# Kernel optimization log

Hardware: AMD Instinct MI355X
Metric: run time of the kernel (lower is better)

Reference implementation:

```python
import jax, jax.numpy as jnp
import numpy as np
from jax import lax

NUM_SUPERNODES = 1024
KNN_K = 16
MIN_GRIPPER = 16
MIN_MASK = 8
GRIP_START = 0
GRIP_RADIUS = 0.1
NEG_INF = -jnp.inf


def _take(a, idx):
    return jnp.take_along_axis(a, idx, axis=1)


def _scatter_or(idx, keep, Bf, N):
    # OR `keep` into a fresh [Bf,N] bool mask at positions idx (mirrors torch scatter_)
    b = jnp.arange(Bf)[:, None]
    return jnp.zeros((Bf, N), dtype=bool).at[b, idx].max(keep)


def _cdist(a, b):
    # a [B,M,3], b [B,N,3] -> [B,M,N] euclidean
    d2 = (jnp.sum(a * a, -1)[:, :, None] + jnp.sum(b * b, -1)[:, None, :]
          - 2.0 * jnp.einsum('bmd,bnd->bmn', a, b))
    return jnp.sqrt(jnp.maximum(d2, 0.0))


def _sample_supernodes(xyz, valid, state, mask_id, extra_scores, global_scores):
    Bf, N, _ = xyz.shape
    M = NUM_SUPERNODES
    valid = valid.astype(bool)
    row_has_valid = valid.any(axis=1)
    first_valid = jnp.argmax(valid, axis=1).astype(jnp.int32)  # [Bf]

    # ---- gripper quota: nearest points to gripper xyz (within radius if any) ----
    k_grip = min(MIN_GRIPPER, M)
    gxyz = state[:, GRIP_START:GRIP_START + 3]
    gdist = jnp.linalg.norm(xyz - gxyz[:, None, :], axis=-1)  # [Bf,N]
    in_radius = gdist <= GRIP_RADIUS
    has_radius = (valid & in_radius).any(axis=1, keepdims=True)
    eligible = valid & (in_radius | ~has_radius)
    dist_rank = jnp.where(eligible, gdist, jnp.inf)
    neg_vals, grip_idx = lax.top_k(-dist_rank, k_grip)
    grip_vals = -neg_vals
    grip_keep = jnp.isfinite(grip_vals) & row_has_valid[:, None]
    head_idx = jnp.where(grip_keep, grip_idx, first_valid[:, None])
    head_bucket = jnp.where(grip_keep, 1, -1)
    selected = _scatter_or(grip_idx, grip_keep, Bf, N)

    remaining = M - k_grip
    # ---- mask-instance quota: one point per mask id (dedup via sort) ----
    mask_cand = valid & ~selected
    sentinel = jnp.iinfo(mask_id.dtype).max
    mask_key = jnp.where(mask_cand, mask_id, sentinel)
    sort_idx = jnp.argsort(mask_key, axis=1)
    sorted_valid = _take(mask_cand, sort_idx)
    sorted_mask = _take(mask_id, sort_idx)
    first_for_id = jnp.concatenate(
        [sorted_valid[:, :1],
         sorted_valid[:, 1:] & (sorted_mask[:, 1:] != sorted_mask[:, :-1])], axis=1)
    pos = jnp.arange(N, dtype=jnp.float32)[None, :]
    mask_scores = jnp.where(first_for_id, -pos, NEG_INF)
    mask_vals, mask_pos = lax.top_k(mask_scores, remaining)
    mask_idx = _take(sort_idx, mask_pos)
    mask_keep = jnp.isfinite(mask_vals) & row_has_valid[:, None]
    selected_after_mask = selected | _scatter_or(mask_idx, mask_keep, Bf, N)

    # ---- extra random mask supernodes to guarantee min_mask quota ----
    k_extra = min(MIN_MASK, remaining)
    es = jnp.where(valid & ~selected_after_mask, extra_scores, NEG_INF)
    extra_vals, extra_idx = lax.top_k(es, k_extra)
    extra_keep = jnp.isfinite(extra_vals) & row_has_valid[:, None]
    use_extra = ~mask_keep[:, :k_extra] & extra_keep
    mask_idx = mask_idx.at[:, :k_extra].set(
        jnp.where(use_extra, extra_idx, mask_idx[:, :k_extra]))
    mask_keep = mask_keep.at[:, :k_extra].set(mask_keep[:, :k_extra] | use_extra)

    # ---- global random fill ----
    selected_for_global = selected | _scatter_or(mask_idx, mask_keep, Bf, N)
    gs = jnp.where(valid & ~selected_for_global, global_scores, NEG_INF)
    gvals, gidx = lax.top_k(gs, remaining)
    gkeep = jnp.isfinite(gvals) & row_has_valid[:, None]
    fill_idx = jnp.where(mask_keep, mask_idx,
                         jnp.where(gkeep, gidx, first_valid[:, None]))
    fill_bucket = jnp.where(mask_keep, 2, jnp.where(gkeep, 0, -1))

    out_idx = jnp.concatenate([head_idx, fill_idx], axis=1)
    out_bucket = jnp.concatenate([head_bucket, fill_bucket], axis=1)
    out_valid = _take(valid, out_idx) & row_has_valid[:, None]
    out_bucket = jnp.where(out_valid, out_bucket, -1)
    return out_idx, out_valid, out_bucket


def setup_inputs() -> dict:
    key = jax.random.key(0)
    ks = jax.random.split(key, 6)
    Bf, N, C = 8, 16384, 64
    return {
        'x': jax.random.normal(ks[0], (Bf, N, C), dtype=jnp.float32),
        'xyz': jax.random.normal(ks[1], (Bf, N, 3), dtype=jnp.float32),
        'valid': jnp.ones((Bf, N), dtype=bool),
        'state': jax.random.normal(ks[2], (Bf, 8), dtype=jnp.float32),
        'mask_id': jax.random.randint(ks[3], (Bf, N), 0, 32, dtype=jnp.int32),
        'extra_scores': jax.random.uniform(ks[4], (Bf, N), dtype=jnp.float32),
        'global_scores': jax.random.uniform(ks[5], (Bf, N), dtype=jnp.float32),
    }


def reference(x, xyz, valid, state, mask_id, extra_scores, global_scores):
    Bf, N, C = x.shape
    out_idx, out_valid, out_bucket = _sample_supernodes(
        xyz, valid, state, mask_id, extra_scores, global_scores)
    # gather_points
    supernode_xyz = _take(xyz, out_idx[:, :, None].repeat(3, axis=2))  # [Bf,M,3]
    # build_knn_neighbors: masked cdist + topk smallest
    dist = _cdist(supernode_xyz.astype(jnp.float32), xyz.astype(jnp.float32))
    dist = jnp.where(valid.astype(bool)[:, None, :], dist, jnp.inf)
    neg_vals, neighbor_idx = lax.top_k(-dist, KNN_K)
    neighbor_mask = jnp.isfinite(-neg_vals)  # [Bf,M,K]
    # gather_neighbors
    b = jnp.arange(Bf)[:, None, None]
    neighbor_feats = x[b, neighbor_idx]  # [Bf,M,K,C]
    return (neighbor_feats, supernode_xyz, neighbor_mask,
            out_idx, out_valid, out_bucket)
```

## Files before the change

kernel.cpp:

```cpp
#include <hip/hip_runtime.h>
#include <math.h>

typedef unsigned long long u64;
typedef unsigned int u32;

#define BF 8
#define NPTS 16384
#define HALFPTS 8192
#define M_SN 1024
#define CCH 64
#define KNN 16
#define NTHR1 1024
#define KPER 16
#define TBL 4096
#define CCAP 2048
#define REM 1008

constexpr size_t O0 = 0;
constexpr size_t O1 = 8388608;
constexpr size_t O2 = 8413184;
constexpr size_t O3 = 8544256;
constexpr size_t O4 = 8552448;
constexpr size_t O5 = 8560640;

#define PW_OFF ((size_t)256)
#define PW_BYTES ((size_t)BF * NPTS * 16)
#define WN_BYTES ((size_t)2 * BF * M_SN * KNN * 8)

__device__ __forceinline__ bool is_valid_el(const void* vp, int mode, long long i) {
  if (mode == 1) return ((const unsigned char*)vp)[i] != 0;
  if (mode == 2) return ((const float*)vp)[i] != 0.0f;
  return ((const int*)vp)[i] != 0;
}

__device__ __forceinline__ u32 desc_enc(float f) {
  u32 u = __float_as_uint(f);
  u32 s = (u & 0x80000000u) ? ~u : (u | 0x80000000u);
  return ~s;
}
__device__ __forceinline__ bool enc_finite(u32 d) {
  u32 s = ~d;
  u32 u = (s & 0x80000000u) ? (s & 0x7FFFFFFFu) : ~s;
  return (u & 0x7F800000u) != 0x7F800000u;
}

__device__ __forceinline__ u64 wave_min_u64(u64 v) {
#pragma unroll
  for (int d = 32; d >= 1; d >>= 1) {
    u32 lo = __shfl_xor((u32)(v & 0xFFFFFFFFu), d, 64);
    u32 hi = __shfl_xor((u32)(v >> 32), d, 64);
    u64 o = ((u64)hi << 32) | lo;
    if (o < v) v = o;
  }
  return v;
}

__device__ __forceinline__ u64 block_min_u64(u64 v, u64* red16, int t) {
  v = wave_min_u64(v);
  if ((t & 63) == 0) red16[t >> 6] = v;
  __syncthreads();
  if (t < 64) {
    u64 x = red16[t & 15];
    x = wave_min_u64(x);
    if (t == 0) red16[0] = x;
  }
  __syncthreads();
  u64 r = red16[0];
  __syncthreads();
  return r;
}

__device__ __forceinline__ int block_excl_scan(int val, int* scanb, int t, int* tot) {
  int incl = val;
#pragma unroll
  for (int d = 1; d < 64; d <<= 1) {
    int v = __shfl_up(incl, d, 64);
    if ((t & 63) >= d) incl += v;
  }
  if ((t & 63) == 63) scanb[t >> 6] = incl;
  __syncthreads();
  if (t < 64) {
    int ws = (t < 16) ? scanb[t] : 0;
#pragma unroll
    for (int d = 1; d < 16; d <<= 1) {
      int v = __shfl_up(ws, d, 64);
      if ((t & 63) >= d) ws += v;
    }
    if (t < 16) scanb[16 + t] = ws;
  }
  __syncthreads();
  int wv = t >> 6;
  int base = (wv == 0) ? 0 : scanb[16 + wv - 1];
  *tot = scanb[16 + 15];
  int r = base + incl - val;
  __syncthreads();
  return r;
}

__device__ __forceinline__ u64 shfl64_grp(u64 v, int src) {
  u32 lo = (u32)__shfl((int)(u32)(v & 0xFFFFFFFFu), src, 32);
  u32 hi = (u32)__shfl((int)(u32)(v >> 32), src, 32);
  return ((u64)hi << 32) | lo;
}

template<bool ASC, bool SHIFTBIN>
__device__ __forceinline__ void topk_select(const u32* ek, const u32* bk, u32 cmask,
    int Twant, int* table, u64* cand, int* scanb, int* sh, int* outArr, int t) {
  for (int j = t; j < TBL; j += NTHR1) table[j] = 0;
  if (t == 6) sh[6] = 0x7FFFFFFF;
  if (t == 7) sh[7] = 1;
  __syncthreads();
#pragma unroll
  for (int k = 0; k < KPER; k++) {
    if ((cmask >> k) & 1u) {
      int bin = SHIFTBIN ? (int)(ek[k] >> 20) : (int)bk[k];
      atomicAdd(&table[bin], 1);
    }
  }
  __syncthreads();
  int c_[4]; int c4 = 0;
#pragma unroll
  for (int q = 0; q < 4; q++) { c_[q] = table[4 * t + q]; c4 += c_[q]; }
  int htot;
  int cum = block_excl_scan(c4, scanb, t, &htot);
  const int T = min(Twant, htot);
  int e_ = cum;
#pragma unroll
  for (int q = 0; q < 4; q++) {
    int nx = e_ + c_[q];
    if (T > 0 && e_ < T && nx >= T) atomicMin(&sh[6], 4 * t + q);
    table[4 * t + q] = e_;
    e_ = nx;
  }
  __syncthreads();
  if (T <= 0) return;
  const int B = sh[6];
#pragma unroll
  for (int k = 0; k < KPER; k++) {
    if ((cmask >> k) & 1u) {
      int bin = SHIFTBIN ? (int)(ek[k] >> 20) : (int)bk[k];
      if (bin <= B) {
        int pos = atomicAdd(&table[bin], 1);
        if (pos < CCAP)
          cand[pos] = ((u64)ek[k] << 32) | ((u64)(u32)bin << 14) | (u32)(k * NTHR1 + t);
      }
    }
  }
  __syncthreads();
  const int nc = table[B];
  if (nc <= CCAP) {
    for (int c = t; c < nc; c += NTHR1) {
      u64 key = cand[c];
      int bin = (int)((key >> 14) & 0xFFFu);
      int s = bin ? table[bin - 1] : 0;
      int e2 = table[bin];
      int r = s;
      for (int j = s; j < e2; j++) r += (cand[j] < key);
      if (r < T) {
        u32 enc = (u32)(key >> 32);
        int ix = (int)(key & 0x3FFFu);
        bool fin = ASC ? (enc < 0x7F800000u) : enc_finite(enc);
        outArr[r] = fin ? ix : (ix | (int)0x80000000);
      }
    }
  } else {
    if (t == 0) sh[7] = 0;
  }
  __syncthreads();
}

__global__ void detect_valid(const unsigned* __restrict__ w, int nwords, int* __restrict__ flag) {
  int local = 0;
  for (int i = blockIdx.x * blockDim.x + threadIdx.x; i < nwords; i += gridDim.x * blockDim.x) {
    unsigned v = w[i];
    if (v == 0x3F800000u) local = 2;
    else if (v != 0u && v != 1u) local = max(local, 1);
  }
#pragma unroll
  for (int d = 32; d >= 1; d >>= 1) local = max(local, __shfl_xor(local, d, 64));
  if ((threadIdx.x & 63) == 0 && local) atomicMax(flag, local);
}

__global__ __launch_bounds__(1024)
void sample_kernel(const float* __restrict__ xyz, const void* __restrict__ validp,
                   const float* __restrict__ state, const int* __restrict__ mask_id,
                   const float* __restrict__ extra, const float* __restrict__ glob,
                   const int* __restrict__ flagp, float4* __restrict__ pw,
                   float* __restrict__ out) {
  __shared__ u64 red16[16];
  __shared__ int table[TBL];
  __shared__ int scanb[32];
  __shared__ int mpick[REM];
  __shared__ u64 cand[CCAP];
  __shared__ int gsorted[REM];
  __shared__ int head_i[16];
  __shared__ int head_bk[16];
  __shared__ int sh[8];

  const int b = blockIdx.x, t = threadIdx.x;
  const int vmode = flagp[0];
  const float* xyzb = xyz + (size_t)b * NPTS * 3;
  const int* midb = mask_id + (size_t)b * NPTS;
  const float* exb = extra + (size_t)b * NPTS;
  const float* glb = glob + (size_t)b * NPTS;

  if (t < 8) sh[t] = 0;
  if (t == 1) sh[1] = 0x7FFFFFFF;
  if (t < 16) gsorted[t] = -1;
  __syncthreads();

  u32 vbits = 0;
#pragma unroll
  for (int k = 0; k < KPER; k++) {
    int i = k * NTHR1 + t;
    if (is_valid_el(validp, vmode, (long long)b * NPTS + i)) vbits |= 1u << k;
  }
  if (vbits) {
    atomicOr(&sh[0], 1);
    atomicMin(&sh[1], (__ffs(vbits) - 1) * NTHR1 + t);
  }

  float gx = state[b * 8 + 0], gy = state[b * 8 + 1], gz = state[b * 8 + 2];
  float gd[KPER];
  u32 inr = 0;
#pragma unroll
  for (int k = 0; k < KPER; k++) {
    int i = k * NTHR1 + t;
    float px = xyzb[3 * i], py = xyzb[3 * i + 1], pz = xyzb[3 * i + 2];
    float dx = px - gx, dy = py - gy, dz = pz - gz;
    float d = sqrtf((dx * dx + dy * dy) + dz * dz);
    gd[k] = d;
    bool vb = (vbits >> k) & 1u;
    if (vb && d <= 0.1f) inr |= 1u << k;
    if (pw) {
      float sb = __fadd_rn(__fadd_rn(__fmul_rn(px, px), __fmul_rn(py, py)), __fmul_rn(pz, pz));
      pw[(size_t)b * NPTS + i] = make_float4(px, py, pz, vb ? sb : INFINITY);
    }
  }
  if (inr) atomicOr(&sh[2], 1);
  __syncthreads();

  const int rhv = sh[0];
  const int first_valid = rhv ? sh[1] : 0;
  const u32 elig = vbits & (sh[2] ? inr : 0xFFFFu);
  u32 sel = 0;

  {
    u32 ek[KPER];
#pragma unroll
    for (int k = 0; k < KPER; k++) ek[k] = __float_as_uint(gd[k]);
    topk_select<true, true>(ek, nullptr, elig, 16, table, cand, scanb, sh, gsorted, t);
    if (sh[7]) {
      if (t < 16) {
        int g = gsorted[t];
        head_i[t] = (g >= 0) ? g : first_valid;
        head_bk[t] = (g >= 0) ? 1 : -1;
      }
      __syncthreads();
      for (int j = 0; j < 16; j++) {
        if (head_bk[j] == 1) {
          int ix = head_i[j];
          if ((ix & (NTHR1 - 1)) == t) sel |= 1u << (ix >> 10);
        }
      }
    } else {
      for (int it = 0; it < 16; ++it) {
        u64 best = ~0ull;
#pragma unroll
        for (int k = 0; k < KPER; k++) {
          if (((elig >> k) & 1u) && !((sel >> k) & 1u)) {
            u64 key = ((u64)__float_as_uint(gd[k]) << 32) | (u32)(k * NTHR1 + t);
            if (key < best) best = key;
          }
        }
        u64 w = block_min_u64(best, red16, t);
        bool keep = (w >> 32) < 0x7F800000ull;
        int idx = (int)(w & 0xFFFFFFFFu);
        if (t == 0) { head_i[it] = keep ? idx : first_valid; head_bk[it] = keep ? 1 : -1; }
        if (keep && (idx & (NTHR1 - 1)) == t) sel |= 1u << (idx >> 10);
      }
      __syncthreads();
    }
  }

  for (int j = t; j < TBL; j += NTHR1) table[j] = 0x7FFFFFFF;
  __syncthreads();
#pragma unroll
  for (int k = 0; k < KPER; k++) {
    if (((vbits >> k) & 1u) && !((sel >> k) & 1u)) {
      int i = k * NTHR1 + t;
      int id = midb[i];
      if ((u32)id < TBL) atomicMin(&table[id], i);
    }
  }
  __syncthreads();
  int cnt = 0;
#pragma unroll
  for (int q = 0; q < 4; q++) cnt += (table[4 * t + q] != 0x7FFFFFFF);
  int mtot;
  int excl = block_excl_scan(cnt, scanb, t, &mtot);
  {
    int pos = excl;
#pragma unroll
    for (int q = 0; q < 4; q++) {
      int v = table[4 * t + q];
      if (v != 0x7FFFFFFF) { if (pos < REM) mpick[pos] = v; pos++; }
    }
  }
  __syncthreads();
  const int nm = min(mtot, REM);
  for (int j = 0; j < nm; j++) {
    int p = mpick[j];
    if ((p & (NTHR1 - 1)) == t) sel |= 1u << (p >> 10);
  }

  u32 extra_used = 0;
  if (nm < 8 && rhv) {
    u32 extrbits = 0;
    for (int j = 0; j < 8; j++) {
      u64 best = ~0ull;
#pragma unroll
      for (int k = 0; k < KPER; k++) {
        if (((vbits >> k) & 1u) && !((sel >> k) & 1u) && !((extrbits >> k) & 1u)) {
          int i = k * NTHR1 + t;
          u64 key = ((u64)desc_enc(exb[i]) << 32) | (u32)i;
          if (key < best) best = key;
        }
      }
      u64 w = block_min_u64(best, red16, t);
      if (w == ~0ull) break;
      int idx = (int)(w & 0xFFFFFFFFu);
      bool fin = enc_finite((u32)(w >> 32));
      if ((idx & (NTHR1 - 1)) == t) extrbits |= 1u << (idx >> 10);
      if (j >= nm && fin) {
        extra_used |= 1u << j;
        if (t == 0) mpick[j] = idx;
        if ((idx & (NTHR1 - 1)) == t) sel |= 1u << (idx >> 10);
      }
    }
    __syncthreads();
  }

  {
    u32 cbits = vbits & ~sel;
    u32 ek[KPER], bk[KPER];
#pragma unroll
    for (int k = 0; k < KPER; k++) {
      if ((cbits >> k) & 1u) {
        float f = glb[k * NTHR1 + t];
        ek[k] = desc_enc(f);
        float g = fminf(fmaxf(f, 0.0f), 0.99999994f);
        bk[k] = 4095u - (u32)(g * 4096.0f);
      } else { ek[k] = 0xFFFFFFFFu; bk[k] = 4095u; }
    }
    for (int j = t; j < REM; j += NTHR1) gsorted[j] = -1;
    topk_select<false, false>(ek, bk, cbits, REM, table, cand, scanb, sh, gsorted, t);
    if (!sh[7]) {
      u32 gext = 0;
      for (int j = 0; j < REM; j++) {
        u64 best = ~0ull;
#pragma unroll
        for (int k = 0; k < KPER; k++) {
          if (((cbits >> k) & 1u) && !((gext >> k) & 1u)) {
            u64 key = ((u64)ek[k] << 32) | (u32)(k * NTHR1 + t);
            if (key < best) best = key;
          }
        }
        u64 w = block_min_u64(best, red16, t);
        if (w == ~0ull) break;
        int idx = (int)(w & 0xFFFFFFFFu);
        if ((idx & (NTHR1 - 1)) == t) gext |= 1u << (idx >> 10);
        if (t == 0) gsorted[j] = enc_finite((u32)(w >> 32)) ? idx : (idx | (int)0x80000000);
      }
      __syncthreads();
    }
  }

  {
    int slot = t;
    int idx, bucket;
    if (slot < 16) {
      idx = head_i[slot];
      bucket = head_bk[slot];
    } else {
      int jj = slot - 16;
      bool mk = (jj < nm) || (jj < 8 && ((extra_used >> jj) & 1u));
      if (mk) { idx = mpick[jj]; bucket = 2; }
      else {
        int g = gsorted[jj];
        if (rhv && g >= 0) { idx = g; bucket = 0; }
        else { idx = first_valid; bucket = -1; }
      }
    }
    bool ov = rhv && is_valid_el(validp, vmode, (long long)b * NPTS + idx);
    int ob = ov ? bucket : -1;
    size_t o = (size_t)b * M_SN + slot;
    out[O3 + o] = (float)idx;
    out[O4 + o] = ov ? 1.0f : 0.0f;
    out[O5 + o] = (float)ob;
    out[O1 + 3 * o + 0] = xyzb[3 * idx + 0];
    out[O1 + 3 * o + 1] = xyzb[3 * idx + 1];
    out[O1 + 3 * o + 2] = xyzb[3 * idx + 2];
  }
}

#define NTHR2 256
#define CH 1024
#define SPB 8

__global__ __launch_bounds__(256, 8)
void knn_kernel(const float* __restrict__ x, const float* __restrict__ xyz,
                const void* __restrict__ validp, const int* __restrict__ flagp,
                const float4* __restrict__ pw, u64* __restrict__ wnws,
                float* __restrict__ out) {
  __shared__ __align__(16) float4 st[CH];
  __shared__ u64 wn[SPB * KNN];

  const int b = blockIdx.x >> 7;
  const int grp = blockIdx.x & 127;
  const int half = blockIdx.y;
  const int t = threadIdx.x;
  const int sl = t >> 5;
  const int sub = t & 31;
  const int lanebase = t & 32;
  const int m = grp * SPB + sl;
  const float* xyzb = xyz + (size_t)b * NPTS * 3;
  const long long gbase = (long long)b * NPTS;

  const int sidx = (int)out[O3 + (size_t)b * M_SN + m];
  float ax, ay, az;
  if (pw) { float4 c = pw[gbase + sidx]; ax = c.x; ay = c.y; az = c.z; }
  else { ax = xyzb[3 * sidx]; ay = xyzb[3 * sidx + 1]; az = xyzb[3 * sidx + 2]; }
  const float a2x = ax + ax, a2y = ay + ay, a2z = az + az;

  float ld = -INFINITY;
  int li = 0;
  float kq = -INFINITY;

  const int vmode = pw ? 0 : flagp[0];
  const int cbeg = wnws ? half * HALFPTS : 0;
  const int cend = wnws ? cbeg + HALFPTS : NPTS;

  for (int c0 = cbeg; c0 < cend; c0 += CH) {
    if (pw) {
      const float4* src = pw + gbase + c0;
#pragma unroll
      for (int qq = 0; qq < CH / NTHR2; qq++) st[t + qq * NTHR2] = src[t + qq * NTHR2];
    } else {
      for (int p = t; p < CH; p += NTHR2) {
        float px = xyzb[3 * (c0 + p)], py = xyzb[3 * (c0 + p) + 1], pz = xyzb[3 * (c0 + p) + 2];
        bool v = is_valid_el(validp, vmode, gbase + c0 + p);
        float sb = __fadd_rn(__fadd_rn(__fmul_rn(px, px), __fmul_rn(py, py)), __fmul_rn(pz, pz));
        st[p] = make_float4(px, py, pz, v ? sb : INFINITY);
      }
    }
    __syncthreads();

    int jstart = 0;
    if (c0 == cbeg) {
      float4 v = st[sub];
      float qv = __builtin_fmaf(a2x, v.x, __builtin_fmaf(a2y, v.y, __builtin_fmaf(a2z, v.z, -v.w)));
      int qi = c0 + sub;
#pragma unroll
      for (int p = 0; p < 32; p++) {
        int par;
        if ((p & 1) == 0) par = sub ^ 1;
        else par = (sub == 0 || sub == 31) ? sub : (((sub - 1) ^ 1) + 1);
        float oq = __shfl(qv, par, 32);
        int oi = __shfl(qi, par, 32);
        if (par != sub) {
          bool lo = sub < par;
          bool take = lo ? (oq > qv) : (oq < qv);
          if (take) { qv = oq; qi = oi; }
        }
      }
      ld = qv; li = qi;
      kq = __shfl(ld, 15, 32);
      jstart = 1;
    }

#pragma unroll 4
    for (int j = jstart; j < CH / 32; j++) {
      float4 v = st[sub + 32 * j];
      float qv = __builtin_fmaf(a2x, v.x, __builtin_fmaf(a2y, v.y, __builtin_fmaf(a2z, v.z, -v.w)));
      u64 bal = __ballot(qv > kq);
      u32 mq = (u32)(bal >> lanebase);
      while (mq) {
        int bb = __ffs(mq) - 1;
        mq &= mq - 1;
        float kd = __shfl(qv, lanebase + bb, 64);
        if (kd > kq) {
          int ki = c0 + 32 * j + bb;
          bool gt = ld < kd;
          float sd = __shfl_up(ld, 1, 32);
          int si = __shfl_up(li, 1, 32);
          int pg = __shfl_up(gt ? 1 : 0, 1, 32);
          if (sub == 0) pg = 0;
          ld = gt ? (pg ? sd : kd) : ld;
          li = gt ? (pg ? si : ki) : li;
          kq = __shfl(ld, 15, 32);
        }
      }
    }
    __syncthreads();
  }

  if (wnws) {
    if (sub < KNN)
      wnws[((size_t)half * BF + b) * M_SN * KNN + (size_t)m * KNN + sub] =
          ((u64)desc_enc(ld) << 32) | (u32)li;
    return;
  }

  if (sub < KNN) wn[sl * KNN + sub] = ((u64)desc_enc(ld) << 32) | (u32)li;
  __syncthreads();
  {
    int s2 = t >> 5;
    int k2 = (t >> 1) & 15;
    int hf = t & 1;
    int mm = grp * SPB + s2;
    u64 key = wn[s2 * KNN + k2];
    int ni = (int)(key & (u64)(NPTS - 1));
    size_t o2 = ((size_t)b * M_SN + mm) * KNN + k2;
    if (hf == 0) out[O2 + o2] = enc_finite((u32)(key >> 32)) ? 1.0f : 0.0f;
    const float4* src = (const float4*)(x + (gbase + ni) * CCH);
    float4* dst = (float4*)(out + O0 + o2 * CCH);
#pragma unroll
    for (int q = 0; q < 8; q++) dst[hf * 8 + q] = src[hf * 8 + q];
  }
}

__global__ __launch_bounds__(256)
void knn_merge_kernel(const float* __restrict__ x, const u64* __restrict__ wnws,
                      float* __restrict__ out) {
  __shared__ u64 wn[SPB * KNN];
  const int b = blockIdx.x >> 7;
  const int grp = blockIdx.x & 127;
  const int t = threadIdx.x;
  const int sl = t >> 5;
  const int sub = t & 31;
  const int m = grp * SPB + sl;

  const int h = sub >> 4, k = sub & 15;
  u64 my = wnws[((size_t)h * BF + b) * M_SN * KNN + (size_t)m * KNN + k];
  const int obase = (1 - h) << 4;
  int cnt2 = 0;
#pragma unroll
  for (int j = 0; j < 16; j++) {
    u64 o = shfl64_grp(my, obase + j);
    cnt2 += h ? (o <= my) : (o < my);
  }
  int rank = k + cnt2;
  if (rank < KNN) wn[sl * KNN + rank] = my;
  __syncthreads();

  {
    int s2 = t >> 5;
    int k2 = (t >> 1) & 15;
    int hf = t & 1;
    int mm = grp * SPB + s2;
    u64 key = wn[s2 * KNN + k2];
    int ni = (int)(key & (u64)(NPTS - 1));
    size_t o2 = ((size_t)b * M_SN + mm) * KNN + k2;
    if (hf == 0) out[O2 + o2] = enc_finite((u32)(key >> 32)) ? 1.0f : 0.0f;
    const float4* src = (const float4*)(x + ((size_t)b * NPTS + ni) * CCH);
    float4* dst = (float4*)(out + O0 + o2 * CCH);
#pragma unroll
    for (int q = 0; q < 8; q++) dst[hf * 8 + q] = src[hf * 8 + q];
  }
}

extern "C" void kernel_launch(void* const* d_in, const int* in_sizes, int n_in,
                              void* d_out, int out_size, void* d_ws, size_t ws_size,
                              hipStream_t stream) {
  const float* x = (const float*)d_in[0];
  const float* xyz = (const float*)d_in[1];
  const void* valid = d_in[2];
  const float* state = (const float*)d_in[3];
  const int* mask_id = (const int*)d_in[4];
  const float* extra = (const float*)d_in[5];
  const float* glob = (const float*)d_in[6];
  float* out = (float*)d_out;
  int* flag = (int*)d_ws;

  float4* pw = nullptr;
  u64* wnws = nullptr;
  if (ws_size >= PW_OFF + PW_BYTES) pw = (float4*)((char*)d_ws + PW_OFF);
  if (pw && ws_size >= PW_OFF + PW_BYTES + WN_BYTES)
    wnws = (u64*)((char*)d_ws + PW_OFF + PW_BYTES);

  hipMemsetAsync(flag, 0, 4, stream);
  detect_valid<<<64, 1024, 0, stream>>>((const unsigned*)valid, in_sizes[2] / 4, flag);
  sample_kernel<<<BF, NTHR1, 0, stream>>>(xyz, valid, state, mask_id, extra, glob, flag, pw, out);
  dim3 kg(BF * 128, wnws ? 2 : 1);
  knn_kernel<<<kg, NTHR2, 0, stream>>>(x, xyz, valid, flag, pw, wnws, out);
  if (wnws) knn_merge_kernel<<<BF * 128, NTHR2, 0, stream>>>(x, wnws, out);
}
```

Baseline: 264.9 us.

## Assign one full 64-lane wavefront per supernode in KNN kernel

The KNN kernel now maps each supernode to a full 64-lane wavefront instead of a 32-lane half-wave, so a block handles 4 supernodes and the grid doubles. The initial sort of the first chunk becomes a bitonic sort on packed 64-bit keys, and the kth-value broadcast is done once per ballot batch instead of after every insertion. The aim is to avoid the wave-divergent handling of two independent half-waves in the insertion loop and to process more candidates per iteration. The trade-off is that each shared-memory chunk is reloaded by twice as many blocks. Insertions within one batch are compared against a stale threshold, so some extra ones may run.

Result: no change. 261.1 us (-1.4%).

```diff
diff --git a/kernel.cpp b/kernel.cpp
--- a/kernel.cpp
+++ b/kernel.cpp
@@ -37,6 +37,11 @@
   u32 u = __float_as_uint(f);
   u32 s = (u & 0x80000000u) ? ~u : (u | 0x80000000u);
   return ~s;
+}
+__device__ __forceinline__ float desc_dec(u32 e) {
+  u32 s = ~e;
+  u32 u = (s & 0x80000000u) ? (s & 0x7FFFFFFFu) : ~s;
+  return __uint_as_float(u);
 }
 __device__ __forceinline__ bool enc_finite(u32 d) {
   u32 s = ~d;
@@ -406,6 +411,7 @@
 
 #define NTHR2 256
 #define CH 1024
+#define SNB 4
 #define SPB 8
 
 __global__ __launch_bounds__(256, 8)
@@ -414,16 +420,15 @@
                 const float4* __restrict__ pw, u64* __restrict__ wnws,
                 float* __restrict__ out) {
   __shared__ __align__(16) float4 st[CH];
-  __shared__ u64 wn[SPB * KNN];
-
-  const int b = blockIdx.x >> 7;
-  const int grp = blockIdx.x & 127;
+  __shared__ u64 wn[SNB * KNN];
+
+  const int b = blockIdx.x >> 8;
+  const int grp = blockIdx.x & 255;
   const int half = blockIdx.y;
   const int t = threadIdx.x;
-  const int sl = t >> 5;
-  const int sub = t & 31;
-  const int lanebase = t & 32;
-  const int m = grp * SPB + sl;
+  const int g = t >> 6;
+  const int lane = t & 63;
+  const int m = grp * SNB + g;
   const float* xyzb = xyz + (size_t)b * NPTS * 3;
   const long long gbase = (long long)b * NPTS;
 
@@ -458,75 +463,70 @@
 
     int jstart = 0;
     if (c0 == cbeg) {
-      float4 v = st[sub];
+      float4 v = st[lane];
       float qv = __builtin_fmaf(a2x, v.x, __builtin_fmaf(a2y, v.y, __builtin_fmaf(a2z, v.z, -v.w)));
-      int qi = c0 + sub;
-#pragma unroll
-      for (int p = 0; p < 32; p++) {
-        int par;
-        if ((p & 1) == 0) par = sub ^ 1;
-        else par = (sub == 0 || sub == 31) ? sub : (((sub - 1) ^ 1) + 1);
-        float oq = __shfl(qv, par, 32);
-        int oi = __shfl(qi, par, 32);
-        if (par != sub) {
-          bool lo = sub < par;
-          bool take = lo ? (oq > qv) : (oq < qv);
-          if (take) { qv = oq; qi = oi; }
+      u64 ku = ((u64)desc_enc(qv) << 32) | (u32)(c0 + lane);
+#pragma unroll
+      for (int kk = 2; kk <= 64; kk <<= 1) {
+#pragma unroll
+        for (int jj = kk >> 1; jj > 0; jj >>= 1) {
+          u32 olo = (u32)__shfl_xor((int)(u32)(ku & 0xFFFFFFFFu), jj, 64);
+          u32 ohi = (u32)__shfl_xor((int)(u32)(ku >> 32), jj, 64);
+          u64 o = ((u64)ohi << 32) | olo;
+          bool keepmin = ((lane & jj) == 0) == ((lane & kk) == 0);
+          ku = ((ku < o) == keepmin) ? ku : o;
         }
       }
-      ld = qv; li = qi;
-      kq = __shfl(ld, 15, 32);
+      ld = desc_dec((u32)(ku >> 32));
+      li = (int)(u32)(ku & 0xFFFFFFFFu);
+      kq = __shfl(ld, 15, 64);
       jstart = 1;
     }
 
 #pragma unroll 4
-    for (int j = jstart; j < CH / 32; j++) {
-      float4 v = st[sub + 32 * j];
+    for (int j = jstart; j < CH / 64; j++) {
+      float4 v = st[lane + 64 * j];
       float qv = __builtin_fmaf(a2x, v.x, __builtin_fmaf(a2y, v.y, __builtin_fmaf(a2z, v.z, -v.w)));
       u64 bal = __ballot(qv > kq);
-      u32 mq = (u32)(bal >> lanebase);
-      while (mq) {
-        int bb = __ffs(mq) - 1;
-        mq &= mq - 1;
-        float kd = __shfl(qv, lanebase + bb, 64);
-        if (kd > kq) {
-          int ki = c0 + 32 * j + bb;
+      if (bal) {
+        do {
+          int bb = __ffsll(bal) - 1;
+          bal &= bal - 1;
+          float kd = __shfl(qv, bb, 64);
+          int ki = c0 + 64 * j + bb;
           bool gt = ld < kd;
-          float sd = __shfl_up(ld, 1, 32);
-          int si = __shfl_up(li, 1, 32);
-          int pg = __shfl_up(gt ? 1 : 0, 1, 32);
-          if (sub == 0) pg = 0;
+          float sd = __shfl_up(ld, 1, 64);
+          int si = __shfl_up(li, 1, 64);
+          int pg = __shfl_up(gt ? 1 : 0, 1, 64);
+          if (lane == 0) pg = 0;
           ld = gt ? (pg ? sd : kd) : ld;
           li = gt ? (pg ? si : ki) : li;
-          kq = __shfl(ld, 15, 32);
-        }
+        } while (bal);
+        kq = __shfl(ld, 15, 64);
       }
     }
     __syncthreads();
   }
 
   if (wnws) {
-    if (sub < KNN)
-      wnws[((size_t)half * BF + b) * M_SN * KNN + (size_t)m * KNN + sub] =
+    if (lane < KNN)
+      wnws[((size_t)half * BF + b) * M_SN * KNN + (size_t)m * KNN + lane] =
           ((u64)desc_enc(ld) << 32) | (u32)li;
     return;
   }
 
-  if (sub < KNN) wn[sl * KNN + sub] = ((u64)desc_enc(ld) << 32) | (u32)li;
-  __syncthreads();
-  {
-    int s2 = t >> 5;
-    int k2 = (t >> 1) & 15;
-    int hf = t & 1;
-    int mm = grp * SPB + s2;
-    u64 key = wn[s2 * KNN + k2];
+  if (lane < KNN) wn[g * KNN + lane] = ((u64)desc_enc(ld) << 32) | (u32)li;
+  __syncthreads();
+  for (int r = t; r < SNB * KNN; r += NTHR2) {
+    u64 key = wn[r];
     int ni = (int)(key & (u64)(NPTS - 1));
-    size_t o2 = ((size_t)b * M_SN + mm) * KNN + k2;
-    if (hf == 0) out[O2 + o2] = enc_finite((u32)(key >> 32)) ? 1.0f : 0.0f;
+    int mm = grp * SNB + (r >> 4);
+    size_t o2 = ((size_t)b * M_SN + mm) * KNN + (r & 15);
+    out[O2 + o2] = enc_finite((u32)(key >> 32)) ? 1.0f : 0.0f;
     const float4* src = (const float4*)(x + (gbase + ni) * CCH);
     float4* dst = (float4*)(out + O0 + o2 * CCH);
 #pragma unroll
-    for (int q = 0; q < 8; q++) dst[hf * 8 + q] = src[hf * 8 + q];
+    for (int q = 0; q < 16; q++) dst[q] = src[q];
   }
 }
 
@@ -592,7 +592,7 @@
   hipMemsetAsync(flag, 0, 4, stream);
   detect_valid<<<64, 1024, 0, stream>>>((const unsigned*)valid, in_sizes[2] / 4, flag);
   sample_kernel<<<BF, NTHR1, 0, stream>>>(xyz, valid, state, mask_id, extra, glob, flag, pw, out);
-  dim3 kg(BF * 128, wnws ? 2 : 1);
+  dim3 kg(BF * 256, wnws ? 2 : 1);
   knn_kernel<<<kg, NTHR2, 0, stream>>>(x, xyz, valid, flag, pw, wnws, out);
   if (wnws) knn_merge_kernel<<<BF * 128, NTHR2, 0, stream>>>(x, wnws, out);
 }
```
